# Kernel tuning notes

Measured on AMD Instinct MI355X. Metric: run time of the kernel, lower is better.

## Reference

```python
import jax, jax.numpy as jnp
import numpy as np

EPS = 1e-8  # torch.nn.CosineSimilarity eps


def setup_inputs() -> dict:
    key = jax.random.key(0)
    k1, k2, k3 = jax.random.split(key, 3)
    C, S, D = 1024, 16, 512
    x = jax.random.normal(k1, (C, S, D), dtype=jnp.float32)
    w = jax.random.normal(k2, (1,), dtype=jnp.float32)
    b = jax.random.normal(k3, (1,), dtype=jnp.float32)
    return {"x": x, "w": w, "b": b}


def reference(x, w, b):
    # stable_ge2e: leave-one-out positive centroids, full negative centroids.
    C, S, D = x.shape
    wp = jax.nn.softplus(w)  # (1,)

    sum_c = x.sum(axis=1)                      # (C, D)
    mean_c = sum_c / S                         # negative centroids (C, D)
    loo = (sum_c[:, None, :] - x) / (S - 1.0)  # leave-one-out centroids (C, S, D)

    nx = jnp.linalg.norm(x, axis=-1)           # (C, S)
    nmean = jnp.linalg.norm(mean_c, axis=-1)   # (C,)
    nloo = jnp.linalg.norm(loo, axis=-1)       # (C, S)

    # cosine similarities (clamped denominator, as in torch CosineSimilarity)
    sim_neg = jnp.einsum('jid,kd->jik', x, mean_c) / jnp.maximum(
        nx[:, :, None] * nmean[None, None, :], EPS)          # (C, S, C)
    sim_pos = jnp.einsum('jid,jid->ji', x, loo) / jnp.maximum(nx * nloo, EPS)  # (C, S)

    # on the diagonal k == j use the leave-one-out positive centroid
    eye = jnp.eye(C, dtype=bool)
    sim = jnp.where(eye[:, None, :], sim_pos[:, :, None], sim_neg)  # (C, S, C)

    logits = wp * sim + b
    logS = jax.nn.log_softmax(logits, axis=-1)
    Sji_j = jnp.einsum('jij->ji', logS)                        # (C, S) diagonal
    Sji_k = jax.scipy.special.logsumexp(logS, axis=-1)         # (C, S) (== 0 post-softmax)
    loss = -(Sji_j - Sji_k).reshape(-1)
    return loss.mean()
```

## Files before the change

kernel.cpp:

```cpp
#include <hip/hip_runtime.h>
#include <math.h>

#define CC 1024
#define SS 16
#define DD 512
#define RR (CC*SS)
#define EPSV 1e-8f
#define LDB 520
#define CHUNK 32

typedef __attribute__((ext_vector_type(8))) short short8;
typedef __attribute__((ext_vector_type(4))) float f32x4;
typedef unsigned short ushort_t;

__device__ __forceinline__ unsigned short f2bf(float f) {
  unsigned u = __float_as_uint(f);
  u += 0x7fffu + ((u >> 16) & 1u);
  return (unsigned short)(u >> 16);
}

__device__ __forceinline__ void async16(void* l, const void* g) {
  __builtin_amdgcn_global_load_lds(
      (const __attribute__((address_space(1))) void*)g,
      (__attribute__((address_space(3))) void*)l, 16, 0, 0);
}

__device__ __forceinline__ float softplusf(float v) {
  return (v > 20.f) ? v : log1pf(expf(v));
}

__global__ __launch_bounds__(256) void k_pre(
    const float* __restrict__ x, ushort_t* __restrict__ mn,
    float* __restrict__ nx, float* __restrict__ simpos,
    ushort_t* __restrict__ xn) {
  __shared__ float xs[SS * DD];
  __shared__ float sums[DD];
  __shared__ float red[4];
  __shared__ float snm;
  __shared__ float rinv[SS];
  const int j = blockIdx.x, tid = threadIdx.x;
  const int wid = tid >> 6, lane = tid & 63;
  const float4* xj = (const float4*)(x + (size_t)j * SS * DD);
  float4* xs4 = (float4*)xs;
#pragma unroll
  for (int t = 0; t < 8; ++t) xs4[tid + t * 256] = xj[tid + t * 256];
  __syncthreads();

  float sx = 0.f, sy = 0.f;
  const float2* xs2 = (const float2*)xs;
#pragma unroll
  for (int i = 0; i < SS; ++i) {
    float2 v = xs2[i * (DD / 2) + tid];
    sx += v.x; sy += v.y;
  }
  ((float2*)sums)[tid] = make_float2(sx, sy);
  const float mxs = sx * (1.0f / SS), mys = sy * (1.0f / SS);
  float m2 = mxs * mxs + mys * mys;
#pragma unroll
  for (int off = 32; off > 0; off >>= 1) m2 += __shfl_xor(m2, off, 64);
  if (lane == 0) red[wid] = m2;
  __syncthreads();
  if (tid == 0) snm = sqrtf(red[0] + red[1] + red[2] + red[3]);
  __syncthreads();
  const float inm = (1.0f / SS) / snm;
  {
    unsigned lo = f2bf(sx * inm), hi = f2bf(sy * inm);
    ((unsigned*)(mn + (size_t)j * DD))[tid] = lo | (hi << 16);
  }

  for (int i = wid; i < SS; i += 4) {
    float nx2 = 0.f, dxs = 0.f, t2 = 0.f;
    const float2* xr2 = (const float2*)(xs + i * DD);
    const float2* sm2 = (const float2*)sums;
#pragma unroll
    for (int d2 = 0; d2 < DD / 2; d2 += 64) {
      float2 xv = xr2[d2 + lane];
      float2 sc = sm2[d2 + lane];
      nx2 = fmaf(xv.x, xv.x, fmaf(xv.y, xv.y, nx2));
      dxs = fmaf(xv.x, sc.x, fmaf(xv.y, sc.y, dxs));
      float tx = sc.x - xv.x, ty = sc.y - xv.y;
      t2 = fmaf(tx, tx, fmaf(ty, ty, t2));
    }
#pragma unroll
    for (int off = 32; off > 0; off >>= 1) {
      nx2 += __shfl_xor(nx2, off, 64);
      dxs += __shfl_xor(dxs, off, 64);
      t2  += __shfl_xor(t2,  off, 64);
    }
    if (lane == 0) {
      float nxv = sqrtf(nx2);
      float tn  = sqrtf(t2);
      float num = (dxs - nx2) * (1.0f / (SS - 1));
      float den = fmaxf(nxv * tn * (1.0f / (SS - 1)), EPSV);
      nx[j * SS + i] = nxv;
      rinv[i] = 1.0f / nxv;
      simpos[j * SS + i] = num / den;
    }
  }
  __syncthreads();
  if (xn) {
    uint2* dst = (uint2*)(xn + (size_t)j * SS * DD);
    const float4* src4 = (const float4*)xs;
#pragma unroll
    for (int t = 0; t < 8; ++t) {
      const int idx = tid + t * 256;
      const float ri = rinv[idx >> 7];
      float4 v = src4[idx];
      uint2 o;
      o.x = (unsigned)f2bf(v.x * ri) | ((unsigned)f2bf(v.y * ri) << 16);
      o.y = (unsigned)f2bf(v.z * ri) | ((unsigned)f2bf(v.w * ri) << 16);
      dst[idx] = o;
    }
  }
}

template <bool USE_XN>
__global__ __launch_bounds__(256, 2) void k_gemm(
    const float* __restrict__ x, const ushort_t* __restrict__ xn,
    const ushort_t* __restrict__ mn, const float* __restrict__ nx,
    const float* __restrict__ simpos, const float* __restrict__ wptr,
    const float* __restrict__ bptr, float* __restrict__ ps) {
  __shared__ ushort_t bs[2][CHUNK * LDB];
  const int tid = threadIdx.x;
  const int wid = tid >> 6, lane = tid & 63;
  const int cL = lane & 15, quad = lane >> 4;
  const int bid = (int)blockIdx.x;
  const int tile = (bid & 7) * 64 + (bid >> 3);
  const int rb = tile >> 2, cb = tile & 3;
  const int r0 = rb * 128, cbase = cb * 256;
  const float wp = softplusf(wptr[0]), bv = bptr[0];

  short8 af[2][16];
  int jw[2];
  float sp[2][4], sacc[2][4];
#pragma unroll
  for (int rt = 0; rt < 2; ++rt) {
    const int row = r0 + wid * 32 + rt * 16 + cL;
    if (USE_XN) {
      const short8* src = (const short8*)(xn + (size_t)row * DD);
#pragma unroll
      for (int kc = 0; kc < 16; ++kc) af[rt][kc] = src[kc * 4 + quad];
    } else {
      const float* xr = x + (size_t)row * DD;
      const float invn = 1.0f / nx[row];
#pragma unroll
      for (int kc = 0; kc < 16; ++kc) {
        const int k0 = kc * 32 + quad * 8;
        float4 p = *(const float4*)(xr + k0);
        float4 q = *(const float4*)(xr + k0 + 4);
        short8 v;
        v[0] = f2bf(p.x * invn); v[1] = f2bf(p.y * invn);
        v[2] = f2bf(p.z * invn); v[3] = f2bf(p.w * invn);
        v[4] = f2bf(q.x * invn); v[5] = f2bf(q.y * invn);
        v[6] = f2bf(q.z * invn); v[7] = f2bf(q.w * invn);
        af[rt][kc] = v;
      }
    }
    jw[rt] = (r0 + wid * 32 + rt * 16) >> 4;
#pragma unroll
    for (int r = 0; r < 4; ++r) {
      sp[rt][r] = simpos[r0 + wid * 32 + rt * 16 + quad * 4 + r];
      sacc[rt][r] = 0.f;
    }
  }

  {
    const ushort_t* gsrc = mn + (size_t)cbase * DD;
#pragma unroll
    for (int t = 0; t < 8; ++t) {
      const int rr = wid + t * 4;
      async16(&bs[0][rr * LDB + lane * 8], gsrc + (size_t)rr * DD + lane * 8);
    }
  }
  __syncthreads();

  for (int cc = 0; cc < 8; ++cc) {
    if (cc < 7) {
      const ushort_t* gsrc = mn + (size_t)(cbase + (cc + 1) * CHUNK) * DD;
      ushort_t* dst = bs[(cc + 1) & 1];
#pragma unroll
      for (int t = 0; t < 8; ++t) {
        const int rr = wid + t * 4;
        async16(&dst[rr * LDB + lane * 8], gsrc + (size_t)rr * DD + lane * 8);
      }
    }
    const ushort_t* B = bs[cc & 1];
    f32x4 acc[2][2];
#pragma unroll
    for (int rt = 0; rt < 2; ++rt)
#pragma unroll
      for (int f = 0; f < 2; ++f) acc[rt][f] = (f32x4){0.f, 0.f, 0.f, 0.f};
#pragma unroll
    for (int kc = 0; kc < 16; ++kc) {
      short8 bfr[2];
#pragma unroll
      for (int f = 0; f < 2; ++f)
        bfr[f] = *(const short8*)&B[(f * 16 + cL) * LDB + kc * 32 + quad * 8];
#pragma unroll
      for (int rt = 0; rt < 2; ++rt)
#pragma unroll
        for (int f = 0; f < 2; ++f)
          acc[rt][f] = __builtin_amdgcn_mfma_f32_16x16x32_bf16(
              af[rt][kc], bfr[f], acc[rt][f], 0, 0, 0);
    }
    const int c0 = cbase + cc * CHUNK;
#pragma unroll
    for (int rt = 0; rt < 2; ++rt)
#pragma unroll
      for (int f = 0; f < 2; ++f) {
        const int cg = c0 + f * 16 + cL;
        const bool diag = (cg == jw[rt]);
#pragma unroll
        for (int r = 0; r < 4; ++r) {
          const float sim = diag ? sp[rt][r] : acc[rt][f][r];
          sacc[rt][r] += __expf(fmaf(wp, sim, bv));
        }
      }
    __syncthreads();
  }

#pragma unroll
  for (int rt = 0; rt < 2; ++rt)
#pragma unroll
    for (int r = 0; r < 4; ++r) {
      float v = sacc[rt][r];
#pragma unroll
      for (int off = 1; off < 16; off <<= 1) v += __shfl_xor(v, off, 64);
      if (cL == 0)
        ps[(size_t)(r0 + wid * 32 + rt * 16 + quad * 4 + r) * 4 + cb] = v;
    }
}

__global__ __launch_bounds__(1024) void k_loss(
    const float* __restrict__ ps, const float* __restrict__ simpos,
    const float* __restrict__ wptr, const float* __restrict__ bptr,
    float* __restrict__ out) {
  __shared__ float red[16];
  const int tid = threadIdx.x;
  const float wp = softplusf(wptr[0]), bv = bptr[0];
  float acc = 0.f;
#pragma unroll
  for (int i = 0; i < RR / 1024; ++i) {
    const int row = i * 1024 + tid;
    const f32x4 v = ((const f32x4*)ps)[row];
    const float s = v[0] + v[1] + v[2] + v[3];
    acc += logf(s) - fmaf(wp, simpos[row], bv);
  }
#pragma unroll
  for (int off = 32; off > 0; off >>= 1) acc += __shfl_xor(acc, off, 64);
  if ((tid & 63) == 0) red[tid >> 6] = acc;
  __syncthreads();
  if (tid < 64) {
    float v = (tid < 16) ? red[tid] : 0.f;
#pragma unroll
    for (int off = 8; off > 0; off >>= 1) v += __shfl_xor(v, off, 64);
    if (tid == 0) out[0] = v * (1.0f / RR);
  }
}

extern "C" void kernel_launch(void* const* d_in, const int* in_sizes, int n_in,
                              void* d_out, int out_size, void* d_ws, size_t ws_size,
                              hipStream_t stream) {
  const float* x = (const float*)d_in[0];
  const float* w = (const float*)d_in[1];
  const float* b = (const float*)d_in[2];
  float* out = (float*)d_out;

  const size_t xn_bytes = (size_t)RR * DD * 2;
  const size_t rest = (size_t)CC * DD * 2 + (size_t)RR * 4 * 2 +
                      (size_t)RR * 4 * 4;
  const bool use_xn = ws_size >= xn_bytes + rest + 256;

  char* base = (char*)d_ws;
  ushort_t* xn = use_xn ? (ushort_t*)base : nullptr;
  char* p = base + (use_xn ? xn_bytes : 0);
  ushort_t* mn = (ushort_t*)p;  p += (size_t)CC * DD * 2;
  float* nx     = (float*)p;    p += (size_t)RR * 4;
  float* simpos = (float*)p;    p += (size_t)RR * 4;
  float* ps     = (float*)p;

  k_pre<<<CC, 256, 0, stream>>>(x, mn, nx, simpos, xn);
  if (use_xn)
    k_gemm<true><<<512, 256, 0, stream>>>(x, xn, mn, nx, simpos, w, b, ps);
  else
    k_gemm<false><<<512, 256, 0, stream>>>(x, xn, mn, nx, simpos, w, b, ps);
  k_loss<<<1, 1024, 0, stream>>>(ps, simpos, w, b, out);
}
```

Baseline: 113.5 us.

## Widen GEMM row tile to 256 and split final loss reduction across blocks

Changes the GEMM tile from 128x256 to 256x128 so each wave holds four 16-row A fragments in registers and reuses each B chunk from LDS across more MFMAs, halving the number of column chunks streamed per block. Partial row sums grow to 8 per row, and the single-block loss kernel is replaced by a 64-block combine kernel plus a tiny final reduction. The larger register footprint (64 short8 A fragments plus accumulators) risks spilling or reduced occupancy under the 2-block launch bound.

After: 143.4 us. 1.26x slower.

```diff
diff --git a/kernel.cpp b/kernel.cpp
--- a/kernel.cpp
+++ b/kernel.cpp
@@ -126,16 +126,17 @@
   const int cL = lane & 15, quad = lane >> 4;
   const int bid = (int)blockIdx.x;
   const int tile = (bid & 7) * 64 + (bid >> 3);
-  const int rb = tile >> 2, cb = tile & 3;
-  const int r0 = rb * 128, cbase = cb * 256;
+  const int rb = tile >> 3, cb = tile & 7;
+  const int r0 = rb * 256, cbase = cb * 128;
   const float wp = softplusf(wptr[0]), bv = bptr[0];
-
-  short8 af[2][16];
-  int jw[2];
-  float sp[2][4], sacc[2][4];
-#pragma unroll
-  for (int rt = 0; rt < 2; ++rt) {
-    const int row = r0 + wid * 32 + rt * 16 + cL;
+  const int row0w = r0 + wid * 64;
+
+  short8 af[4][16];
+  int jw[4];
+  float sp[4][4], sacc[4][4];
+#pragma unroll
+  for (int rt = 0; rt < 4; ++rt) {
+    const int row = row0w + rt * 16 + cL;
     if (USE_XN) {
       const short8* src = (const short8*)(xn + (size_t)row * DD);
 #pragma unroll
@@ -156,10 +157,10 @@
         af[rt][kc] = v;
       }
     }
-    jw[rt] = (r0 + wid * 32 + rt * 16) >> 4;
+    jw[rt] = (row0w + rt * 16) >> 4;
 #pragma unroll
     for (int r = 0; r < 4; ++r) {
-      sp[rt][r] = simpos[r0 + wid * 32 + rt * 16 + quad * 4 + r];
+      sp[rt][r] = simpos[row0w + rt * 16 + quad * 4 + r];
       sacc[rt][r] = 0.f;
     }
   }
@@ -174,8 +175,8 @@
   }
   __syncthreads();
 
-  for (int cc = 0; cc < 8; ++cc) {
-    if (cc < 7) {
+  for (int cc = 0; cc < 4; ++cc) {
+    if (cc < 3) {
       const ushort_t* gsrc = mn + (size_t)(cbase + (cc + 1) * CHUNK) * DD;
       ushort_t* dst = bs[(cc + 1) & 1];
 #pragma unroll
@@ -185,9 +186,9 @@
       }
     }
     const ushort_t* B = bs[cc & 1];
-    f32x4 acc[2][2];
-#pragma unroll
-    for (int rt = 0; rt < 2; ++rt)
+    f32x4 acc[4][2];
+#pragma unroll
+    for (int rt = 0; rt < 4; ++rt)
 #pragma unroll
       for (int f = 0; f < 2; ++f) acc[rt][f] = (f32x4){0.f, 0.f, 0.f, 0.f};
 #pragma unroll
@@ -197,7 +198,7 @@
       for (int f = 0; f < 2; ++f)
         bfr[f] = *(const short8*)&B[(f * 16 + cL) * LDB + kc * 32 + quad * 8];
 #pragma unroll
-      for (int rt = 0; rt < 2; ++rt)
+      for (int rt = 0; rt < 4; ++rt)
 #pragma unroll
         for (int f = 0; f < 2; ++f)
           acc[rt][f] = __builtin_amdgcn_mfma_f32_16x16x32_bf16(
@@ -205,7 +206,7 @@
     }
     const int c0 = cbase + cc * CHUNK;
 #pragma unroll
-    for (int rt = 0; rt < 2; ++rt)
+    for (int rt = 0; rt < 4; ++rt)
 #pragma unroll
       for (int f = 0; f < 2; ++f) {
         const int cg = c0 + f * 16 + cL;
@@ -220,42 +221,43 @@
   }
 
 #pragma unroll
-  for (int rt = 0; rt < 2; ++rt)
+  for (int rt = 0; rt < 4; ++rt)
 #pragma unroll
     for (int r = 0; r < 4; ++r) {
       float v = sacc[rt][r];
 #pragma unroll
       for (int off = 1; off < 16; off <<= 1) v += __shfl_xor(v, off, 64);
       if (cL == 0)
-        ps[(size_t)(r0 + wid * 32 + rt * 16 + quad * 4 + r) * 4 + cb] = v;
-    }
-}
-
-__global__ __launch_bounds__(1024) void k_loss(
+        ps[(size_t)(row0w + rt * 16 + quad * 4 + r) * 8 + cb] = v;
+    }
+}
+
+__global__ __launch_bounds__(256) void k_combine(
     const float* __restrict__ ps, const float* __restrict__ simpos,
     const float* __restrict__ wptr, const float* __restrict__ bptr,
-    float* __restrict__ out) {
-  __shared__ float red[16];
+    float* __restrict__ p2) {
+  __shared__ float red[4];
   const int tid = threadIdx.x;
+  const int row = blockIdx.x * 256 + tid;
   const float wp = softplusf(wptr[0]), bv = bptr[0];
-  float acc = 0.f;
-#pragma unroll
-  for (int i = 0; i < RR / 1024; ++i) {
-    const int row = i * 1024 + tid;
-    const f32x4 v = ((const f32x4*)ps)[row];
-    const float s = v[0] + v[1] + v[2] + v[3];
-    acc += logf(s) - fmaf(wp, simpos[row], bv);
-  }
-#pragma unroll
-  for (int off = 32; off > 0; off >>= 1) acc += __shfl_xor(acc, off, 64);
-  if ((tid & 63) == 0) red[tid >> 6] = acc;
-  __syncthreads();
-  if (tid < 64) {
-    float v = (tid < 16) ? red[tid] : 0.f;
-#pragma unroll
-    for (int off = 8; off > 0; off >>= 1) v += __shfl_xor(v, off, 64);
-    if (tid == 0) out[0] = v * (1.0f / RR);
-  }
+  const f32x4 a = ((const f32x4*)ps)[row * 2];
+  const f32x4 c = ((const f32x4*)ps)[row * 2 + 1];
+  const float s = (a[0] + a[1] + a[2] + a[3]) + (c[0] + c[1] + c[2] + c[3]);
+  float v = logf(s) - fmaf(wp, simpos[row], bv);
+#pragma unroll
+  for (int off = 32; off > 0; off >>= 1) v += __shfl_xor(v, off, 64);
+  if ((tid & 63) == 0) red[tid >> 6] = v;
+  __syncthreads();
+  if (tid == 0) p2[blockIdx.x] = red[0] + red[1] + red[2] + red[3];
+}
+
+__global__ __launch_bounds__(64) void k_fin(const float* __restrict__ p2,
+                                            float* __restrict__ out) {
+  const int tid = threadIdx.x;
+  float v = p2[tid];
+#pragma unroll
+  for (int off = 32; off > 0; off >>= 1) v += __shfl_xor(v, off, 64);
+  if (tid == 0) out[0] = v * (1.0f / RR);
 }
 
 extern "C" void kernel_launch(void* const* d_in, const int* in_sizes, int n_in,
@@ -268,7 +270,7 @@
 
   const size_t xn_bytes = (size_t)RR * DD * 2;
   const size_t rest = (size_t)CC * DD * 2 + (size_t)RR * 4 * 2 +
-                      (size_t)RR * 4 * 4;
+                      (size_t)RR * 8 * 4 + 64 * 4;
   const bool use_xn = ws_size >= xn_bytes + rest + 256;
 
   char* base = (char*)d_ws;
@@ -277,12 +279,14 @@
   ushort_t* mn = (ushort_t*)p;  p += (size_t)CC * DD * 2;
   float* nx     = (float*)p;    p += (size_t)RR * 4;
   float* simpos = (float*)p;    p += (size_t)RR * 4;
-  float* ps     = (float*)p;
+  float* ps     = (float*)p;    p += (size_t)RR * 8 * 4;
+  float* p2     = (float*)p;
 
   k_pre<<<CC, 256, 0, stream>>>(x, mn, nx, simpos, xn);
   if (use_xn)
     k_gemm<true><<<512, 256, 0, stream>>>(x, xn, mn, nx, simpos, w, b, ps);
   else
     k_gemm<false><<<512, 256, 0, stream>>>(x, xn, mn, nx, simpos, w, b, ps);
-  k_loss<<<1, 1024, 0, stream>>>(ps, simpos, w, b, out);
-}
+  k_combine<<<RR / 256, 256, 0, stream>>>(ps, simpos, w, b, p2);
+  k_fin<<<1, 64, 0, stream>>>(p2, out);
+}
```
